# Kernel tuning notes

Measured on AMD Instinct MI355X. Metric: run time of the kernel, lower is better.

The kernel has to match this reference:

```python
import jax, jax.numpy as jnp
import numpy as np

HIDDEN = 2048
NUM_HEADS = 16
NUM_KV_HEADS = 8
HEAD_DIM = 128
EPS = 1e-6
ROPE_THETA = 10000.0
SEQ = 2048
Q_SIZE = NUM_HEADS * HEAD_DIM
KV_SIZE = NUM_KV_HEADS * HEAD_DIM


def rmsnorm_f32(x, w, eps=EPS):
    # RMSNormF32: normalize in float32, scale by weight
    xf = x.astype(jnp.float32)
    var = jnp.mean(xf * xf, axis=-1, keepdims=True)
    return xf * jax.lax.rsqrt(var + eps) * w.astype(jnp.float32)


def apply_rope(x, cos, sin):
    # x: [S, H, D]; cos/sin: [S, D//2] (neox-style half split)
    half = x.shape[-1] // 2
    x1, x2 = x[..., :half], x[..., half:]
    c = cos[:, None, :]
    s = sin[:, None, :]
    return jnp.concatenate([x1 * c - x2 * s, x2 * c + x1 * s], axis=-1)


def setup_inputs() -> dict:
    key = jax.random.key(0)
    ks = jax.random.split(key, 6)
    return {
        "positions": jnp.arange(SEQ, dtype=jnp.int32),
        "hidden_states": jax.random.normal(ks[0], (SEQ, HIDDEN), jnp.float32),
        "ln_weight": 1.0 + 0.1 * jax.random.normal(ks[1], (HIDDEN,), jnp.float32),
        "qkv_weight": 0.02 * jax.random.normal(ks[2], (Q_SIZE + 2 * KV_SIZE, HIDDEN), jnp.float32),
        "q_norm_weight": 1.0 + 0.1 * jax.random.normal(ks[3], (HEAD_DIM,), jnp.float32),
        "k_norm_weight": 1.0 + 0.1 * jax.random.normal(ks[4], (HEAD_DIM,), jnp.float32),
        "o_weight": 0.02 * jax.random.normal(ks[5], (HIDDEN, Q_SIZE), jnp.float32),
    }


def reference(positions, hidden_states, ln_weight, qkv_weight, q_norm_weight, k_norm_weight, o_weight):
    S = hidden_states.shape[0]
    # 1. input RMSNorm (f32)
    normalized = rmsnorm_f32(hidden_states, ln_weight)
    # 2. fused QKV projection (no bias)
    qkv = normalized @ qkv_weight.T  # [S, q_size + 2*kv_size]
    q = qkv[:, :Q_SIZE].reshape(S, NUM_HEADS, HEAD_DIM)
    k = qkv[:, Q_SIZE:Q_SIZE + KV_SIZE].reshape(S, NUM_KV_HEADS, HEAD_DIM)
    v = qkv[:, Q_SIZE + KV_SIZE:].reshape(S, NUM_KV_HEADS, HEAD_DIM)
    # 3. RoPE (neox half-split, cache built from theta)
    inv_freq = ROPE_THETA ** (-jnp.arange(0, HEAD_DIM, 2, dtype=jnp.float32) / HEAD_DIM)
    freqs = positions.astype(jnp.float32)[:, None] * inv_freq[None, :]  # [S, D/2]
    cos, sin = jnp.cos(freqs), jnp.sin(freqs)
    q = apply_rope(q, cos, sin)
    k = apply_rope(k, cos, sin)
    # 4. per-head q/k RMSNorm (applied after RoPE, as in source)
    q = rmsnorm_f32(q, q_norm_weight)
    k = rmsnorm_f32(k, k_norm_weight)
    # 5. GQA expand kv heads
    rep = NUM_HEADS // NUM_KV_HEADS
    k = jnp.repeat(k, rep, axis=1)  # [S, NH, D]
    v = jnp.repeat(v, rep, axis=1)
    # 6. naive causal attention
    scores = jnp.einsum('shd,thd->hst', q, k) / (HEAD_DIM ** 0.5)  # [NH, S, S]
    causal = jnp.triu(jnp.ones((S, S), dtype=bool), k=1)
    scores = jnp.where(causal[None, :, :], -jnp.inf, scores)
    attn = jax.nn.softmax(scores, axis=-1)
    attn = jnp.nan_to_num(attn, nan=0.0)
    out = jnp.einsum('hst,thd->shd', attn, v).reshape(S, Q_SIZE)
    # 7. output projection
    return out @ o_weight.T
```

## Files before the change

### kernel.cpp

```cpp
#include <hip/hip_runtime.h>
#include <hip/hip_bf16.h>
#include <stdint.h>

typedef unsigned short u16;
typedef __attribute__((ext_vector_type(4))) float f32x4;
typedef __attribute__((ext_vector_type(8))) __bf16 bf16x8;
typedef __attribute__((ext_vector_type(8))) unsigned short u16x8;
typedef __attribute__((ext_vector_type(4))) unsigned short u16x4;

#define SEQ 2048
#define HID 2048
#define HD  128

__device__ __forceinline__ float b2f(u16 v) {
    union { float f; unsigned u; } c; c.u = ((unsigned)v) << 16; return c.f;
}
__device__ __forceinline__ u16 f2b(float f) {
    union { float f; unsigned u; } c; c.f = f;
    unsigned r = c.u + 0x7fffu + ((c.u >> 16) & 1u);
    return (u16)(r >> 16);
}
__device__ __forceinline__ bf16x8 tob(u16x8 v) {
    union { u16x8 u; bf16x8 b; } c; c.u = v; return c.b;
}
__device__ __forceinline__ u16x8 ld8(const u16* p) { return *(const u16x8*)p; }

typedef const __attribute__((address_space(1))) unsigned int* gas_ptr;
typedef __attribute__((address_space(3))) unsigned int* las_ptr;
__device__ __forceinline__ void gld16(const void* g, void* l) {
    __builtin_amdgcn_global_load_lds((gas_ptr)g, (las_ptr)l, 16, 0, 0);
}

__global__ __launch_bounds__(256) void k_prep(const float* __restrict__ x,
                                              const float* __restrict__ w,
                                              u16* __restrict__ normed,
                                              const float* __restrict__ qkvw,
                                              u16* __restrict__ qkvwb) {
    const int b = blockIdx.x, t = threadIdx.x;
    if (b < 2048) {
        const int row = b;
        const float* xr = x + (size_t)row * HID + t * 8;
        f32x4 xa = *(const f32x4*)xr;
        f32x4 xb = *(const f32x4*)(xr + 4);
        float xf[8]; float ss = 0.f;
#pragma unroll
        for (int e = 0; e < 4; ++e) { xf[e] = xa[e]; xf[e + 4] = xb[e]; }
#pragma unroll
        for (int e = 0; e < 8; ++e) ss += xf[e] * xf[e];
#pragma unroll
        for (int m = 32; m; m >>= 1) ss += __shfl_xor(ss, m);
        __shared__ float red[4];
        if ((t & 63) == 0) red[t >> 6] = ss;
        __syncthreads();
        ss = red[0] + red[1] + red[2] + red[3];
        const float sc = rsqrtf(ss * (1.0f / HID) + 1e-6f);
        f32x4 wa = *(const f32x4*)(w + t * 8);
        f32x4 wb = *(const f32x4*)(w + t * 8 + 4);
        u16x8 ov;
#pragma unroll
        for (int e = 0; e < 4; ++e) {
            ov[e] = f2b(xf[e] * sc * wa[e]);
            ov[e + 4] = f2b(xf[e + 4] * sc * wb[e]);
        }
        *(u16x8*)(normed + (size_t)row * HID + t * 8) = ov;
    } else {
        const size_t i = ((size_t)(b - 2048) * 256 + t) * 8;
        f32x4 a = *(const f32x4*)(qkvw + i);
        f32x4 bb = *(const f32x4*)(qkvw + i + 4);
        u16x8 o;
#pragma unroll
        for (int e = 0; e < 4; ++e) { o[e] = f2b(a[e]); o[e + 4] = f2b(bb[e]); }
        *(u16x8*)(qkvwb + i) = o;
    }
}

#define STAGE_G(buf, k0)                                                      \
    do {                                                                      \
        char* a0 = (char*)&As[buf][0][0] + wave * 1024;                       \
        char* a1 = (char*)&As[buf][1][0] + wave * 1024;                       \
        char* b0 = (char*)&Bs[buf][0][0] + wave * 1024;                       \
        char* b1 = (char*)&Bs[buf][1][0] + wave * 1024;                       \
        gld16(ga + (k0), a0);                                                 \
        gld16(ga + (k0) + rowskip, a0 + 4096);                                \
        gld16(ga + (k0) + 32, a1);                                            \
        gld16(ga + (k0) + 32 + rowskip, a1 + 4096);                           \
        gld16(gb + (k0), b0);                                                 \
        gld16(gb + (k0) + rowskip, b0 + 4096);                                \
        gld16(gb + (k0) + 32, b1);                                            \
        gld16(gb + (k0) + 32 + rowskip, b1 + 4096);                           \
    } while (0)

#define GEMM_PIPE(nk)                                                         \
    STAGE_G(0, 0);                                                            \
    for (int t = 0; t < (nk); ++t) {                                          \
        const int cur = t & 1;                                                \
        if (t + 1 < (nk)) {                                                   \
            STAGE_G(cur ^ 1, (t + 1) * 64);                                   \
            asm volatile("s_waitcnt vmcnt(8)" ::: "memory");                  \
        } else {                                                              \
            asm volatile("s_waitcnt vmcnt(0)" ::: "memory");                  \
        }                                                                     \
        __builtin_amdgcn_s_barrier();                                         \
        asm volatile("" ::: "memory");                                       \
        _Pragma("unroll")                                                     \
        for (int h = 0; h < 2; ++h) {                                         \
            const u16* as = &As[cur][h][0];                                   \
            const u16* bs = &Bs[cur][h][0];                                   \
            bf16x8 af[4], bfr[4];                                             \
            _Pragma("unroll")                                                 \
            for (int i = 0; i < 4; ++i)                                       \
                af[i] = tob(ld8(as + (wm * 64 + i * 16 + l16) * 32 + ((quad ^ sw) << 3))); \
            _Pragma("unroll")                                                 \
            for (int j = 0; j < 4; ++j)                                       \
                bfr[j] = tob(ld8(bs + (wn * 64 + j * 16 + l16) * 32 + ((quad ^ sw) << 3))); \
            _Pragma("unroll")                                                 \
            for (int i = 0; i < 4; ++i)                                       \
                _Pragma("unroll")                                             \
                for (int j = 0; j < 4; ++j)                                   \
                    acc[i][j] = __builtin_amdgcn_mfma_f32_16x16x32_bf16(af[i], bfr[j], acc[i][j], 0, 0, 0); \
        }                                                                     \
        asm volatile("" ::: "memory");                                       \
        __builtin_amdgcn_s_barrier();                                        \
    }

__global__ __launch_bounds__(256) void k_gemm_qkv(const u16* __restrict__ A,
                                                  const u16* __restrict__ B,
                                                  u16* __restrict__ qraw,
                                                  u16* __restrict__ kraw,
                                                  u16* __restrict__ vtr,
                                                  int K) {
    __shared__ u16 As[2][2][128 * 32];
    __shared__ u16 Bs[2][2][128 * 32];
    const int tid = threadIdx.x;
    const int wave = tid >> 6, lane = tid & 63, quad = lane >> 4, l16 = lane & 15;
    const int wm = wave >> 1, wn = wave & 1;
    const int sw = (l16 >> 1) & 3;
    const int m0 = blockIdx.x * 128, n0 = blockIdx.y * 128;
    f32x4 acc[4][4];
#pragma unroll
    for (int i = 0; i < 4; ++i)
#pragma unroll
        for (int j = 0; j < 4; ++j) acc[i][j] = (f32x4){0.f, 0.f, 0.f, 0.f};

    const int gchunk = (tid & 3) ^ ((tid >> 3) & 3);
    const u16* ga = A + (size_t)(m0 + (tid >> 2)) * K + gchunk * 8;
    const u16* gb = B + (size_t)(n0 + (tid >> 2)) * K + gchunk * 8;
    const size_t rowskip = (size_t)64 * K;

    GEMM_PIPE(K >> 6)

#pragma unroll
    for (int i = 0; i < 4; ++i) {
        const int row = m0 + wm * 64 + i * 16 + quad * 4;
#pragma unroll
        for (int j = 0; j < 4; ++j) {
            const int col = n0 + wn * 64 + j * 16 + l16;
#pragma unroll
            for (int r = 0; r < 4; ++r) {
                const u16 val = f2b(acc[i][j][r]);
                const int s = row + r;
                if (col < 2048) {
                    const int head = col >> 7, d = col & 127;
                    qraw[((size_t)head * SEQ + s) * HD + d] = val;
                } else if (col < 3072) {
                    const int c = col - 2048, kv = c >> 7, d = c & 127;
                    kraw[((size_t)kv * SEQ + s) * HD + d] = val;
                } else {
                    const int c = col - 3072, kv = c >> 7, d = c & 127;
                    vtr[(size_t)kv * HD * SEQ + (size_t)d * SEQ + s] = val;
                }
            }
        }
    }
}

__global__ __launch_bounds__(256) void k_gemm_of(const u16* __restrict__ A,
                                                 const u16* __restrict__ B,
                                                 float* __restrict__ C,
                                                 int N, int K) {
    __shared__ u16 As[2][2][128 * 32];
    __shared__ u16 Bs[2][2][64 * 32];
    const int tid = threadIdx.x;
    const int wave = tid >> 6, lane = tid & 63, quad = lane >> 4, l16 = lane & 15;
    const int wm = wave >> 1, wn = wave & 1;
    const int sw = (l16 >> 1) & 3;
    const int m0 = blockIdx.x * 128, n0 = blockIdx.y * 64;
    f32x4 acc[4][2];
#pragma unroll
    for (int i = 0; i < 4; ++i)
#pragma unroll
        for (int j = 0; j < 2; ++j) acc[i][j] = (f32x4){0.f, 0.f, 0.f, 0.f};

    const int gchunk = (tid & 3) ^ ((tid >> 3) & 3);
    const u16* ga = A + (size_t)(m0 + (tid >> 2)) * K + gchunk * 8;
    const u16* gb = B + (size_t)(n0 + (tid >> 2)) * K + gchunk * 8;
    const size_t rowskip = (size_t)64 * K;

#define STAGE_OF(buf, k0)                                                     \
    do {                                                                      \
        char* a0 = (char*)&As[buf][0][0] + wave * 1024;                       \
        char* a1 = (char*)&As[buf][1][0] + wave * 1024;                       \
        char* b0 = (char*)&Bs[buf][0][0] + wave * 1024;                       \
        char* b1 = (char*)&Bs[buf][1][0] + wave * 1024;                       \
        gld16(ga + (k0), a0);                                                 \
        gld16(ga + (k0) + rowskip, a0 + 4096);                                \
        gld16(ga + (k0) + 32, a1);                                            \
        gld16(ga + (k0) + 32 + rowskip, a1 + 4096);                           \
        gld16(gb + (k0), b0);                                                 \
        gld16(gb + (k0) + 32, b1);                                            \
    } while (0)

    STAGE_OF(0, 0);
    const int nk = K >> 6;
    for (int t = 0; t < nk; ++t) {
        const int cur = t & 1;
        if (t + 1 < nk) {
            STAGE_OF(cur ^ 1, (t + 1) * 64);
            asm volatile("s_waitcnt vmcnt(6)" ::: "memory");
        } else {
            asm volatile("s_waitcnt vmcnt(0)" ::: "memory");
        }
        __builtin_amdgcn_s_barrier();
        asm volatile("" ::: "memory");
#pragma unroll
        for (int h = 0; h < 2; ++h) {
            const u16* as = &As[cur][h][0];
            const u16* bs = &Bs[cur][h][0];
            bf16x8 af[4], bfr[2];
#pragma unroll
            for (int i = 0; i < 4; ++i)
                af[i] = tob(ld8(as + (wm * 64 + i * 16 + l16) * 32 + ((quad ^ sw) << 3)));
#pragma unroll
            for (int j = 0; j < 2; ++j)
                bfr[j] = tob(ld8(bs + (wn * 32 + j * 16 + l16) * 32 + ((quad ^ sw) << 3)));
#pragma unroll
            for (int i = 0; i < 4; ++i)
#pragma unroll
                for (int j = 0; j < 2; ++j)
                    acc[i][j] = __builtin_amdgcn_mfma_f32_16x16x32_bf16(af[i], bfr[j], acc[i][j], 0, 0, 0);
        }
        asm volatile("" ::: "memory");
        __builtin_amdgcn_s_barrier();
    }
#undef STAGE_OF

#pragma unroll
    for (int i = 0; i < 4; ++i) {
        const int row = m0 + wm * 64 + i * 16 + quad * 4;
#pragma unroll
        for (int j = 0; j < 2; ++j) {
            const int col = n0 + wn * 32 + j * 16 + l16;
#pragma unroll
            for (int r = 0; r < 4; ++r)
                C[(size_t)(row + r) * N + col] = acc[i][j][r];
        }
    }
}

__global__ __launch_bounds__(256) void k_ropeconv(const int* __restrict__ pos,
                                                  const float* __restrict__ qw,
                                                  const float* __restrict__ kw,
                                                  u16* __restrict__ qraw,
                                                  u16* __restrict__ kraw,
                                                  const float* __restrict__ ow,
                                                  u16* __restrict__ owb) {
    if (blockIdx.y < 6) {
        const int s = blockIdx.x;
        const int h = blockIdx.y * 4 + (threadIdx.x >> 6);
        const int d = threadIdx.x & 63;
        const bool isq = h < 16;
        u16* row = isq ? (qraw + ((size_t)h * SEQ + s) * HD)
                       : (kraw + ((size_t)(h - 16) * SEQ + s) * HD);
        const float x1 = b2f(row[d]), x2 = b2f(row[d + 64]);
        const float p = (float)pos[s];
        const float inv = exp2f(-(float)d * (2.0f / 128.0f) * 13.287712379549449f);
        const float fr = p * inv;
        const float c = cosf(fr), sn = sinf(fr);
        const float o1 = x1 * c - x2 * sn;
        const float o2 = x2 * c + x1 * sn;
        float ss = o1 * o1 + o2 * o2;
#pragma unroll
        for (int m = 32; m; m >>= 1) ss += __shfl_xor(ss, m);
        const float sc = rsqrtf(ss * (1.0f / HD) + 1e-6f);
        const float* w = isq ? qw : kw;
        row[d] = f2b(o1 * sc * w[d]);
        row[d + 64] = f2b(o2 * sc * w[d + 64]);
    } else {
        const size_t i = ((size_t)blockIdx.x * 256 + threadIdx.x) * 8;
        f32x4 a = *(const f32x4*)(ow + i);
        f32x4 b = *(const f32x4*)(ow + i + 4);
        u16x8 o;
#pragma unroll
        for (int e = 0; e < 4; ++e) { o[e] = f2b(a[e]); o[e + 4] = f2b(b[e]); }
        *(u16x8*)(owb + i) = o;
    }
}

__global__ __launch_bounds__(256, 4) void k_attn(const u16* __restrict__ qh,
                                                 const u16* __restrict__ kh,
                                                 const u16* __restrict__ vt,
                                                 u16* __restrict__ out,
                                                 u16* __restrict__ po,
                                                 float* __restrict__ pl) {
    const int tid = threadIdx.x;
    const int wave = tid >> 6, lane = tid & 63, quad = lane >> 4, l16 = lane & 15;
    const int head = blockIdx.y;
    const int b = blockIdx.x;
    int qt, part, np;
    if (b < 11)      { qt = b;                      part = 0;            np = 1; }
    else if (b < 33) { qt = 11 + ((b - 11) >> 1);   part = (b - 11) & 1; np = 2; }
    else             { qt = 22 + (b - 33) / 3;      part = (b - 33) % 3; np = 3; }
    const int kvh = head >> 1;
    const int q0 = qt * 64;
    const int ntiles = qt + 1;

    __shared__ u16 Ks[64 * 128];
    __shared__ u16 Vts[128 * 64];
    __shared__ u16 Ps[4][16 * 64];

    const u16* qbase = qh + ((size_t)head * SEQ + q0 + wave * 16) * HD;
    bf16x8 aq[4];
#pragma unroll
    for (int kk = 0; kk < 4; ++kk)
        aq[kk] = tob(ld8(qbase + l16 * HD + kk * 32 + quad * 8));

    f32x4 acco[8];
#pragma unroll
    for (int j = 0; j < 8; ++j) acco[j] = (f32x4){0.f, 0.f, 0.f, 0.f};
    float lsum = 0.f;

    const float sc = 0.08838834764831845f;
    const u16* kbase = kh + (size_t)kvh * SEQ * HD;
    const u16* vbase = vt + (size_t)kvh * HD * SEQ;
    u16* pw = &Ps[wave][0];
    const int qrow_g = q0 + wave * 16 + l16;

    const u16* kg0 = kbase + (size_t)tid * 8;
    const u16* vg0 = vbase + (size_t)(tid >> 3) * SEQ + (size_t)(tid & 7) * 8;
    int kst[4], vst[4];
#pragma unroll
    for (int r = 0; r < 4; ++r) {
        const int krow = r * 16 + (tid >> 4);
        kst[r] = krow * 128 + (((tid & 15) ^ (krow & 7)) << 3);
        const int vrow = r * 32 + (tid >> 3);
        vst[r] = vrow * 64 + (((tid & 7) ^ (vrow & 7)) << 3);
    }

    u16x8 kreg[4], vreg[4];
    {
        const size_t koff = (size_t)part * 64;
#pragma unroll
        for (int r = 0; r < 4; ++r) {
            kreg[r] = ld8(kg0 + koff * HD + (size_t)r * 2048);
            vreg[r] = ld8(vg0 + koff + (size_t)r * 32 * SEQ);
        }
#pragma unroll
        for (int r = 0; r < 4; ++r) {
            *(u16x8*)(&Ks[0] + kst[r]) = kreg[r];
            *(u16x8*)(&Vts[0] + vst[r]) = vreg[r];
        }
    }
    __syncthreads();

    for (int kt = part; kt < ntiles; kt += np) {
        const bool havenext = (kt + np) < ntiles;
        if (havenext) {
            const size_t koff = (size_t)(kt + np) * 64;
#pragma unroll
            for (int r = 0; r < 4; ++r) {
                kreg[r] = ld8(kg0 + koff * HD + (size_t)r * 2048);
                vreg[r] = ld8(vg0 + koff + (size_t)r * 32 * SEQ);
            }
        }

        f32x4 accs[4];
#pragma unroll
        for (int j = 0; j < 4; ++j) accs[j] = (f32x4){0.f, 0.f, 0.f, 0.f};
#pragma unroll
        for (int kk = 0; kk < 4; ++kk) {
#pragma unroll
            for (int j = 0; j < 4; ++j) {
                const int krow = j * 16 + l16;
                const bf16x8 bk = tob(ld8(&Ks[0] + krow * 128 + (((kk * 4 + quad) ^ (krow & 7)) << 3)));
                accs[j] = __builtin_amdgcn_mfma_f32_16x16x32_bf16(bk, aq[kk], accs[j], 0, 0, 0);
            }
        }

        const int k0 = kt * 64;
#pragma unroll
        for (int j = 0; j < 4; ++j) {
            u16x4 pk;
#pragma unroll
            for (int r = 0; r < 4; ++r) {
                const int kpos = k0 + j * 16 + quad * 4 + r;
                const float pv = (kpos > qrow_g) ? 0.f : __expf(accs[j][r] * sc);
                lsum += pv;
                pk[r] = f2b(pv);
            }
            const int blk = (j * 2 + (quad >> 1)) ^ (l16 & 7);
            *(u16x4*)(pw + l16 * 64 + (blk << 3) + ((quad & 1) << 2)) = pk;
        }

#pragma unroll
        for (int kk = 0; kk < 2; ++kk) {
            const bf16x8 ap = tob(ld8(pw + l16 * 64 + (((kk * 4 + quad) ^ (l16 & 7)) << 3)));
#pragma unroll
            for (int j = 0; j < 8; ++j) {
                const int vrow = j * 16 + l16;
                const bf16x8 bv = tob(ld8(&Vts[0] + vrow * 64 + (((kk * 4 + quad) ^ (vrow & 7)) << 3)));
                acco[j] = __builtin_amdgcn_mfma_f32_16x16x32_bf16(ap, bv, acco[j], 0, 0, 0);
            }
        }

        __syncthreads();
        if (havenext) {
#pragma unroll
            for (int r = 0; r < 4; ++r) {
                *(u16x8*)(&Ks[0] + kst[r]) = kreg[r];
                *(u16x8*)(&Vts[0] + vst[r]) = vreg[r];
            }
        }
        __syncthreads();
    }

    float v = lsum;
    v += __shfl_xor(v, 16);
    v += __shfl_xor(v, 32);
    const int rowb = q0 + wave * 16 + quad * 4;

    if (np == 1) {
        f32x4 il;
#pragma unroll
        for (int r = 0; r < 4; ++r) il[r] = 1.0f / __shfl(v, quad * 4 + r);
#pragma unroll
        for (int j = 0; j < 8; ++j) {
            const int col = head * HD + j * 16 + l16;
#pragma unroll
            for (int r = 0; r < 4; ++r)
                out[(size_t)(rowb + r) * 2048 + col] = f2b(acco[j][r] * il[r]);
        }
    } else {
        u16* pob = po + (size_t)part * SEQ * 2048;
        float* plb = pl + (size_t)part * 16 * SEQ;
        if (lane < 16) plb[head * SEQ + q0 + wave * 16 + l16] = v;
#pragma unroll
        for (int j = 0; j < 8; ++j) {
            const int col = head * HD + j * 16 + l16;
#pragma unroll
            for (int r = 0; r < 4; ++r)
                pob[(size_t)(rowb + r) * 2048 + col] = f2b(acco[j][r]);
        }
    }
}

__global__ __launch_bounds__(256) void k_amerge(const u16* __restrict__ po,
                                                const float* __restrict__ pl,
                                                u16* __restrict__ out) {
    const int s = blockIdx.x + 704;
    const int qt = s >> 6;
    const int np = (qt > 21) ? 3 : 2;
    const int t = threadIdx.x;
    const int head = t >> 4;

    float l = 0.f;
#pragma unroll
    for (int p = 0; p < 3; ++p)
        if (p < np) l += pl[(size_t)p * 16 * SEQ + head * SEQ + s];
    const float il = 1.0f / l;

    float o[8] = {0.f, 0.f, 0.f, 0.f, 0.f, 0.f, 0.f, 0.f};
#pragma unroll
    for (int p = 0; p < 3; ++p) {
        if (p < np) {
            const u16x8 vv = ld8(po + (size_t)p * SEQ * 2048 + (size_t)s * 2048 + t * 8);
#pragma unroll
            for (int e = 0; e < 8; ++e) o[e] += b2f(vv[e]);
        }
    }
    u16x8 ov;
#pragma unroll
    for (int e = 0; e < 8; ++e) ov[e] = f2b(o[e] * il);
    *(u16x8*)(out + (size_t)s * 2048 + t * 8) = ov;
}

extern "C" void kernel_launch(void* const* d_in, const int* in_sizes, int n_in,
                              void* d_out, int out_size, void* d_ws, size_t ws_size,
                              hipStream_t stream) {
    const int*   positions = (const int*)d_in[0];
    const float* hidden   = (const float*)d_in[1];
    const float* lnw      = (const float*)d_in[2];
    const float* qkvw     = (const float*)d_in[3];
    const float* qnw      = (const float*)d_in[4];
    const float* knw      = (const float*)d_in[5];
    const float* ow       = (const float*)d_in[6];
    float* outp = (float*)d_out;

    char* ws = (char*)d_ws;
    const size_t MB = 1024ull * 1024ull;
    u16* normed = (u16*)(ws + 0 * MB);
    u16* qraw   = (u16*)(ws + 8 * MB);
    u16* kraw   = (u16*)(ws + 16 * MB);
    u16* vtr    = (u16*)(ws + 20 * MB);
    u16* qkvwb  = (u16*)(ws + 24 * MB);
    u16* owb    = (u16*)(ws + 0 * MB);
    u16* attno  = (u16*)(ws + 24 * MB);
    u16* po     = (u16*)(ws + 32 * MB);
    float* pl   = (float*)(ws + 56 * MB);

    k_prep    <<<6144, 256, 0, stream>>>(hidden, lnw, normed, qkvw, qkvwb);
    k_gemm_qkv<<<dim3(16, 32), 256, 0, stream>>>(normed, qkvwb, qraw, kraw, vtr, HID);
    k_ropeconv<<<dim3(SEQ, 7), 256, 0, stream>>>(positions, qnw, knw, qraw, kraw, ow, owb);
    k_attn    <<<dim3(63, 16), 256, 0, stream>>>(qraw, kraw, vtr, attno, po, pl);
    k_amerge  <<<1344, 256, 0, stream>>>(po, pl, attno);
    k_gemm_of <<<dim3(16, 32), 256, 0, stream>>>(attno, owb, outp, HID, HID);
}
```

Baseline: 246.7 us.

## Keep P in registers via permuted K layout, add 4-way KV split

The K tile rows are permuted when stored to shared memory so that the QK^T MFMA output lands directly in the A-operand layout needed by the PV MFMA. This lets the probability fragments stay in registers, removing the per-wave shared-memory round trip for P and its LDS buffer. The causal work split is also rebalanced into 1/2/3/4-part KV partitions over 80 blocks per head, and occupancy is raised to 5 blocks per CU. The partial-output buffers are compacted to cover only the last 1536 rows, and the merge kernel now handles up to four partials. The costs are more merge traffic and added register pressure from the higher occupancy bound.

```diff
diff --git a/kernel.cpp b/kernel.cpp
--- a/kernel.cpp
+++ b/kernel.cpp
@@ -296,7 +296,7 @@
     }
 }
 
-__global__ __launch_bounds__(256, 4) void k_attn(const u16* __restrict__ qh,
+__global__ __launch_bounds__(256, 5) void k_attn(const u16* __restrict__ qh,
                                                  const u16* __restrict__ kh,
                                                  const u16* __restrict__ vt,
                                                  u16* __restrict__ out,
@@ -307,16 +307,16 @@
     const int head = blockIdx.y;
     const int b = blockIdx.x;
     int qt, part, np;
-    if (b < 11)      { qt = b;                      part = 0;            np = 1; }
-    else if (b < 33) { qt = 11 + ((b - 11) >> 1);   part = (b - 11) & 1; np = 2; }
-    else             { qt = 22 + (b - 33) / 3;      part = (b - 33) % 3; np = 3; }
+    if (b < 8)       { qt = b;                    part = 0;            np = 1; }
+    else if (b < 24) { qt = 8 + ((b - 8) >> 1);   part = (b - 8) & 1;  np = 2; }
+    else if (b < 48) { qt = 16 + (b - 24) / 3;    part = (b - 24) % 3; np = 3; }
+    else             { qt = 24 + ((b - 48) >> 2); part = (b - 48) & 3; np = 4; }
     const int kvh = head >> 1;
     const int q0 = qt * 64;
     const int ntiles = qt + 1;
 
     __shared__ u16 Ks[64 * 128];
     __shared__ u16 Vts[128 * 64];
-    __shared__ u16 Ps[4][16 * 64];
 
     const u16* qbase = qh + ((size_t)head * SEQ + q0 + wave * 16) * HD;
     bf16x8 aq[4];
@@ -332,7 +332,6 @@
     const float sc = 0.08838834764831845f;
     const u16* kbase = kh + (size_t)kvh * SEQ * HD;
     const u16* vbase = vt + (size_t)kvh * HD * SEQ;
-    u16* pw = &Ps[wave][0];
     const int qrow_g = q0 + wave * 16 + l16;
 
     const u16* kg0 = kbase + (size_t)tid * 8;
@@ -340,8 +339,9 @@
     int kst[4], vst[4];
 #pragma unroll
     for (int r = 0; r < 4; ++r) {
-        const int krow = r * 16 + (tid >> 4);
-        kst[r] = krow * 128 + (((tid & 15) ^ (krow & 7)) << 3);
+        const int kp = r * 16 + (tid >> 4);
+        const int u = (kp & 35) | ((kp & 4) << 2) | ((kp & 24) >> 1);
+        kst[r] = u * 128 + (((tid & 15) ^ (u & 7)) << 3);
         const int vrow = r * 32 + (tid >> 3);
         vst[r] = vrow * 64 + (((tid & 7) ^ (vrow & 7)) << 3);
     }
@@ -387,23 +387,21 @@
         }
 
         const int k0 = kt * 64;
+        u16x8 apk[2];
 #pragma unroll
         for (int j = 0; j < 4; ++j) {
-            u16x4 pk;
 #pragma unroll
             for (int r = 0; r < 4; ++r) {
-                const int kpos = k0 + j * 16 + quad * 4 + r;
+                const int kpos = k0 + ((j >> 1) << 5) + (quad << 3) + ((j & 1) << 2) + r;
                 const float pv = (kpos > qrow_g) ? 0.f : __expf(accs[j][r] * sc);
                 lsum += pv;
-                pk[r] = f2b(pv);
+                apk[j >> 1][((j & 1) << 2) + r] = f2b(pv);
             }
-            const int blk = (j * 2 + (quad >> 1)) ^ (l16 & 7);
-            *(u16x4*)(pw + l16 * 64 + (blk << 3) + ((quad & 1) << 2)) = pk;
         }
 
 #pragma unroll
         for (int kk = 0; kk < 2; ++kk) {
-            const bf16x8 ap = tob(ld8(pw + l16 * 64 + (((kk * 4 + quad) ^ (l16 & 7)) << 3)));
+            const bf16x8 ap = tob(apk[kk]);
 #pragma unroll
             for (int j = 0; j < 8; ++j) {
                 const int vrow = j * 16 + l16;
@@ -440,15 +438,15 @@
                 out[(size_t)(rowb + r) * 2048 + col] = f2b(acco[j][r] * il[r]);
         }
     } else {
-        u16* pob = po + (size_t)part * SEQ * 2048;
-        float* plb = pl + (size_t)part * 16 * SEQ;
-        if (lane < 16) plb[head * SEQ + q0 + wave * 16 + l16] = v;
+        u16* pob = po + (size_t)part * (1536 * 2048);
+        float* plb = pl + (size_t)part * (16 * 1536) + (size_t)head * 1536;
+        if (lane < 16) plb[q0 + wave * 16 + l16 - 512] = v;
 #pragma unroll
         for (int j = 0; j < 8; ++j) {
             const int col = head * HD + j * 16 + l16;
 #pragma unroll
             for (int r = 0; r < 4; ++r)
-                pob[(size_t)(rowb + r) * 2048 + col] = f2b(acco[j][r]);
+                pob[(size_t)(rowb + r - 512) * 2048 + col] = f2b(acco[j][r]);
         }
     }
 }
@@ -456,23 +454,23 @@
 __global__ __launch_bounds__(256) void k_amerge(const u16* __restrict__ po,
                                                 const float* __restrict__ pl,
                                                 u16* __restrict__ out) {
-    const int s = blockIdx.x + 704;
+    const int s = blockIdx.x + 512;
     const int qt = s >> 6;
-    const int np = (qt > 21) ? 3 : 2;
+    const int np = (qt >= 24) ? 4 : (qt >= 16) ? 3 : 2;
     const int t = threadIdx.x;
     const int head = t >> 4;
 
     float l = 0.f;
 #pragma unroll
-    for (int p = 0; p < 3; ++p)
-        if (p < np) l += pl[(size_t)p * 16 * SEQ + head * SEQ + s];
+    for (int p = 0; p < 4; ++p)
+        if (p < np) l += pl[(size_t)p * (16 * 1536) + (size_t)head * 1536 + (s - 512)];
     const float il = 1.0f / l;
 
     float o[8] = {0.f, 0.f, 0.f, 0.f, 0.f, 0.f, 0.f, 0.f};
 #pragma unroll
-    for (int p = 0; p < 3; ++p) {
+    for (int p = 0; p < 4; ++p) {
         if (p < np) {
-            const u16x8 vv = ld8(po + (size_t)p * SEQ * 2048 + (size_t)s * 2048 + t * 8);
+            const u16x8 vv = ld8(po + (size_t)p * (1536 * 2048) + (size_t)(s - 512) * 2048 + t * 8);
 #pragma unroll
             for (int e = 0; e < 8; ++e) o[e] += b2f(vv[e]);
         }
@@ -510,7 +508,7 @@
     k_prep    <<<6144, 256, 0, stream>>>(hidden, lnw, normed, qkvw, qkvwb);
     k_gemm_qkv<<<dim3(16, 32), 256, 0, stream>>>(normed, qkvwb, qraw, kraw, vtr, HID);
     k_ropeconv<<<dim3(SEQ, 7), 256, 0, stream>>>(positions, qnw, knw, qraw, kraw, ow, owb);
-    k_attn    <<<dim3(63, 16), 256, 0, stream>>>(qraw, kraw, vtr, attno, po, pl);
-    k_amerge  <<<1344, 256, 0, stream>>>(po, pl, attno);
+    k_attn    <<<dim3(80, 16), 256, 0, stream>>>(qraw, kraw, vtr, attno, po, pl);
+    k_amerge  <<<1536, 256, 0, stream>>>(po, pl, attno);
     k_gemm_of <<<dim3(16, 32), 256, 0, stream>>>(attno, owb, outp, HID, HID);
 }
```

After: 316.0 us. +28.1%, slower.
